# Performance work log

Measured on AMD Instinct MI355X. Metric: run time of the kernel, lower is better.

## Reference

```python
import jax, jax.numpy as jnp
import numpy as np

S, B, F = 2048, 64, 512


def setup_inputs() -> dict:
    key = jax.random.key(0)
    k1, k2 = jax.random.split(key)
    x = jax.random.normal(k1, (S, B, F), dtype=jnp.float32)
    # lengths in [1, S] so every sequence has at least one valid step
    lengths = jax.random.randint(k2, (B,), 1, S + 1, dtype=jnp.int64)
    return {"x": x, "lengths": lengths}


def reference(x, lengths):
    """x: (S, B, F), lengths: (B,) -> (B, 3*F) = [last, mean, max]."""
    s, b, f = x.shape
    # last valid timestep per sequence (extract_last equivalent)
    last = x[lengths - 1, jnp.arange(b), :]                      # (B, F)
    # validity mask over time: (S, B, 1)
    mask = (jnp.arange(s)[:, None] < lengths[None, :])[:, :, None]
    xm = jnp.where(mask, x, 0.0)
    mean = jnp.sum(xm, axis=0) / lengths[:, None].astype(x.dtype)  # (B, F)
    mx = jnp.max(jnp.where(mask, x, -jnp.inf), axis=0)             # (B, F)
    return jnp.concatenate([last, mean, mx], axis=-1)              # (B, 3F)
```

## Files before the change

kernel.cpp:

```cpp
#include <hip/hip_runtime.h>
#include <hip/hip_bf16.h>
#include <math.h>

#define S_DIM 2048
#define B_DIM 64
#define F_DIM 512
#define NCHUNK 128

__device__ __forceinline__ ushort bf16_bits(float v) {
    __hip_bfloat16 h = __float2bfloat16(v);
    return *reinterpret_cast<ushort*>(&h);
}
__device__ __forceinline__ float bf16_val(ushort u) {
    __hip_bfloat16 h = *reinterpret_cast<__hip_bfloat16*>(&u);
    return __bfloat162float(h);
}

__global__ __launch_bounds__(128) void scp_partial(const float* __restrict__ x,
                                                   const int* __restrict__ lengths,
                                                   ushort* __restrict__ ws) {
    const int c = blockIdx.x;
    const int b = blockIdx.y;
    const int f = threadIdx.x * 4;
    const int len = lengths[b];

    const int nj = (len > c) ? ((len - c + NCHUNK - 1) >> 7) : 0;
    if (nj == 0) return;

    float4 sum = make_float4(0.f, 0.f, 0.f, 0.f);
    float4 mx = make_float4(-INFINITY, -INFINITY, -INFINITY, -INFINITY);

    const size_t row_stride = (size_t)B_DIM * F_DIM;
    const float* p = x + (size_t)c * row_stride + (size_t)b * F_DIM + f;
    const size_t step = (size_t)NCHUNK * row_stride;

    #pragma unroll 4
    for (int j = 0; j < nj; ++j) {
        float4 v = *reinterpret_cast<const float4*>(p);
        sum.x += v.x; sum.y += v.y; sum.z += v.z; sum.w += v.w;
        mx.x = fmaxf(mx.x, v.x);
        mx.y = fmaxf(mx.y, v.y);
        mx.z = fmaxf(mx.z, v.z);
        mx.w = fmaxf(mx.w, v.w);
        p += step;
    }

    ushort* dst = ws + ((size_t)b * NCHUNK + c) * (2 * F_DIM);
    ushort4 us, um;
    us.x = bf16_bits(sum.x); us.y = bf16_bits(sum.y);
    us.z = bf16_bits(sum.z); us.w = bf16_bits(sum.w);
    um.x = bf16_bits(mx.x);  um.y = bf16_bits(mx.y);
    um.z = bf16_bits(mx.z);  um.w = bf16_bits(mx.w);
    *reinterpret_cast<ushort4*>(dst + f) = us;
    *reinterpret_cast<ushort4*>(dst + F_DIM + f) = um;
}

__global__ __launch_bounds__(256) void scp_finalize(const float* __restrict__ x,
                                                    const int* __restrict__ lengths,
                                                    const ushort* __restrict__ ws,
                                                    float* __restrict__ out) {
    const int b = blockIdx.x;
    const int y = blockIdx.y;
    const int tid = threadIdx.x;
    const int f4l = tid & 31;
    const int cpar = tid >> 5;
    const int f = y * 128 + f4l * 4;
    const int len = lengths[b];
    const int ncc = (len < NCHUNK) ? len : NCHUNK;

    const float4 last = *reinterpret_cast<const float4*>(
        x + ((size_t)(len - 1) * B_DIM + b) * F_DIM + f);

    float4 sum = make_float4(0.f, 0.f, 0.f, 0.f);
    float4 mx = make_float4(-INFINITY, -INFINITY, -INFINITY, -INFINITY);

    for (int c = cpar; c < ncc; c += 8) {
        const ushort* src = ws + ((size_t)b * NCHUNK + c) * (2 * F_DIM);
        ushort4 s4 = *reinterpret_cast<const ushort4*>(src + f);
        ushort4 m4 = *reinterpret_cast<const ushort4*>(src + F_DIM + f);
        sum.x += bf16_val(s4.x); sum.y += bf16_val(s4.y);
        sum.z += bf16_val(s4.z); sum.w += bf16_val(s4.w);
        mx.x = fmaxf(mx.x, bf16_val(m4.x));
        mx.y = fmaxf(mx.y, bf16_val(m4.y));
        mx.z = fmaxf(mx.z, bf16_val(m4.z));
        mx.w = fmaxf(mx.w, bf16_val(m4.w));
    }

    __shared__ float4 ssum[8][32];
    __shared__ float4 smax[8][32];
    ssum[cpar][f4l] = sum;
    smax[cpar][f4l] = mx;
    __syncthreads();

    if (cpar == 0) {
        #pragma unroll
        for (int k = 1; k < 8; ++k) {
            float4 s4 = ssum[k][f4l];
            float4 m4 = smax[k][f4l];
            sum.x += s4.x; sum.y += s4.y; sum.z += s4.z; sum.w += s4.w;
            mx.x = fmaxf(mx.x, m4.x);
            mx.y = fmaxf(mx.y, m4.y);
            mx.z = fmaxf(mx.z, m4.z);
            mx.w = fmaxf(mx.w, m4.w);
        }

        const float inv = 1.0f / (float)len;
        float4 mean = make_float4(sum.x * inv, sum.y * inv, sum.z * inv, sum.w * inv);

        float* ob = out + (size_t)b * (3 * F_DIM);
        *reinterpret_cast<float4*>(ob + f) = last;
        *reinterpret_cast<float4*>(ob + F_DIM + f) = mean;
        *reinterpret_cast<float4*>(ob + 2 * F_DIM + f) = mx;
    }
}

extern "C" void kernel_launch(void* const* d_in, const int* in_sizes, int n_in,
                              void* d_out, int out_size, void* d_ws, size_t ws_size,
                              hipStream_t stream) {
    const float* x = (const float*)d_in[0];
    const int* lengths = (const int*)d_in[1];
    float* out = (float*)d_out;
    ushort* ws = (ushort*)d_ws;

    scp_partial<<<dim3(NCHUNK, B_DIM), 128, 0, stream>>>(x, lengths, ws);
    scp_finalize<<<dim3(B_DIM, 4), 256, 0, stream>>>(x, lengths, ws, out);
}
```

Measured before the change: 34.33 us.

## Write last timestep from partial kernel and widen finalize grid with tree reduction

The partial kernel now writes the last valid timestep straight to the output from the chunk that holds it, reusing the final loaded vector, so finalize no longer does a scattered read of x. Finalize doubles its grid to 8 feature slices, uses 16 chunk lanes per block, and combines them with a shared-memory tree reduction. This gives the short finalize stage more parallelism, at the cost of extra barriers.

Result: faster. 32.53 us (-5.3%).

```diff
diff --git a/kernel.cpp b/kernel.cpp
--- a/kernel.cpp
+++ b/kernel.cpp
@@ -18,7 +18,8 @@
 
 __global__ __launch_bounds__(128) void scp_partial(const float* __restrict__ x,
                                                    const int* __restrict__ lengths,
-                                                   ushort* __restrict__ ws) {
+                                                   ushort* __restrict__ ws,
+                                                   float* __restrict__ out) {
     const int c = blockIdx.x;
     const int b = blockIdx.y;
     const int f = threadIdx.x * 4;
@@ -29,6 +30,7 @@
 
     float4 sum = make_float4(0.f, 0.f, 0.f, 0.f);
     float4 mx = make_float4(-INFINITY, -INFINITY, -INFINITY, -INFINITY);
+    float4 v  = make_float4(0.f, 0.f, 0.f, 0.f);
 
     const size_t row_stride = (size_t)B_DIM * F_DIM;
     const float* p = x + (size_t)c * row_stride + (size_t)b * F_DIM + f;
@@ -36,13 +38,17 @@
 
     #pragma unroll 4
     for (int j = 0; j < nj; ++j) {
-        float4 v = *reinterpret_cast<const float4*>(p);
+        v = *reinterpret_cast<const float4*>(p);
         sum.x += v.x; sum.y += v.y; sum.z += v.z; sum.w += v.w;
         mx.x = fmaxf(mx.x, v.x);
         mx.y = fmaxf(mx.y, v.y);
         mx.z = fmaxf(mx.z, v.z);
         mx.w = fmaxf(mx.w, v.w);
         p += step;
+    }
+
+    if (c == ((len - 1) & (NCHUNK - 1))) {
+        *reinterpret_cast<float4*>(out + (size_t)b * (3 * F_DIM) + f) = v;
     }
 
     ushort* dst = ws + ((size_t)b * NCHUNK + c) * (2 * F_DIM);
@@ -55,26 +61,22 @@
     *reinterpret_cast<ushort4*>(dst + F_DIM + f) = um;
 }
 
-__global__ __launch_bounds__(256) void scp_finalize(const float* __restrict__ x,
-                                                    const int* __restrict__ lengths,
+__global__ __launch_bounds__(256) void scp_finalize(const int* __restrict__ lengths,
                                                     const ushort* __restrict__ ws,
                                                     float* __restrict__ out) {
     const int b = blockIdx.x;
     const int y = blockIdx.y;
     const int tid = threadIdx.x;
-    const int f4l = tid & 31;
-    const int cpar = tid >> 5;
-    const int f = y * 128 + f4l * 4;
+    const int f4l = tid & 15;
+    const int cpar = tid >> 4;
+    const int f = y * 64 + f4l * 4;
     const int len = lengths[b];
     const int ncc = (len < NCHUNK) ? len : NCHUNK;
-
-    const float4 last = *reinterpret_cast<const float4*>(
-        x + ((size_t)(len - 1) * B_DIM + b) * F_DIM + f);
 
     float4 sum = make_float4(0.f, 0.f, 0.f, 0.f);
     float4 mx = make_float4(-INFINITY, -INFINITY, -INFINITY, -INFINITY);
 
-    for (int c = cpar; c < ncc; c += 8) {
+    for (int c = cpar; c < ncc; c += 16) {
         const ushort* src = ws + ((size_t)b * NCHUNK + c) * (2 * F_DIM);
         ushort4 s4 = *reinterpret_cast<const ushort4*>(src + f);
         ushort4 m4 = *reinterpret_cast<const ushort4*>(src + F_DIM + f);
@@ -86,31 +88,38 @@
         mx.w = fmaxf(mx.w, bf16_val(m4.w));
     }
 
-    __shared__ float4 ssum[8][32];
-    __shared__ float4 smax[8][32];
+    __shared__ float4 ssum[16][16];
+    __shared__ float4 smax[16][16];
     ssum[cpar][f4l] = sum;
     smax[cpar][f4l] = mx;
     __syncthreads();
 
+    #pragma unroll
+    for (int h = 8; h >= 1; h >>= 1) {
+        if (cpar < h) {
+            float4 s4 = ssum[cpar + h][f4l];
+            float4 m4 = smax[cpar + h][f4l];
+            float4 a = ssum[cpar][f4l];
+            float4 m = smax[cpar][f4l];
+            a.x += s4.x; a.y += s4.y; a.z += s4.z; a.w += s4.w;
+            m.x = fmaxf(m.x, m4.x);
+            m.y = fmaxf(m.y, m4.y);
+            m.z = fmaxf(m.z, m4.z);
+            m.w = fmaxf(m.w, m4.w);
+            ssum[cpar][f4l] = a;
+            smax[cpar][f4l] = m;
+        }
+        __syncthreads();
+    }
+
     if (cpar == 0) {
-        #pragma unroll
-        for (int k = 1; k < 8; ++k) {
-            float4 s4 = ssum[k][f4l];
-            float4 m4 = smax[k][f4l];
-            sum.x += s4.x; sum.y += s4.y; sum.z += s4.z; sum.w += s4.w;
-            mx.x = fmaxf(mx.x, m4.x);
-            mx.y = fmaxf(mx.y, m4.y);
-            mx.z = fmaxf(mx.z, m4.z);
-            mx.w = fmaxf(mx.w, m4.w);
-        }
-
+        float4 a = ssum[0][f4l];
+        float4 m = smax[0][f4l];
         const float inv = 1.0f / (float)len;
-        float4 mean = make_float4(sum.x * inv, sum.y * inv, sum.z * inv, sum.w * inv);
-
         float* ob = out + (size_t)b * (3 * F_DIM);
-        *reinterpret_cast<float4*>(ob + f) = last;
-        *reinterpret_cast<float4*>(ob + F_DIM + f) = mean;
-        *reinterpret_cast<float4*>(ob + 2 * F_DIM + f) = mx;
+        *reinterpret_cast<float4*>(ob + F_DIM + f) =
+            make_float4(a.x * inv, a.y * inv, a.z * inv, a.w * inv);
+        *reinterpret_cast<float4*>(ob + 2 * F_DIM + f) = m;
     }
 }
 
@@ -122,6 +131,6 @@
     float* out = (float*)d_out;
     ushort* ws = (ushort*)d_ws;
 
-    scp_partial<<<dim3(NCHUNK, B_DIM), 128, 0, stream>>>(x, lengths, ws);
-    scp_finalize<<<dim3(B_DIM, 4), 256, 0, stream>>>(x, lengths, ws, out);
+    scp_partial<<<dim3(NCHUNK, B_DIM), 128, 0, stream>>>(x, lengths, ws, out);
+    scp_finalize<<<dim3(B_DIM, 8), 256, 0, stream>>>(lengths, ws, out);
 }
```
